# Optimization experiments

Hardware: AMD Instinct MI355X
Metric: run time of the kernel (lower is better)

The kernel has to match this reference:

```python
import jax, jax.numpy as jnp
import numpy as np

BIOSYNTHETIC_FAMILIES = {'glutamate': ['E','Q','P','R','K'], 'aspartate': ['D','N','T','I','M','K'], 'serine': ['S','G','C'], 'pyruvate': ['A','V','L'], 'aromatic': ['F','Y','W'], 'histidine': ['H']}
CODON_TABLE = {'UUU':'F','UUC':'F','UUA':'L','UUG':'L','CUU':'L','CUC':'L','CUA':'L','CUG':'L','AUU':'I','AUC':'I','AUA':'I','AUG':'M','GUU':'V','GUC':'V','GUA':'V','GUG':'V','UCU':'S','UCC':'S','UCA':'S','UCG':'S','CCU':'P','CCC':'P','CCA':'P','CCG':'P','ACU':'T','ACC':'T','ACA':'T','ACG':'T','GCU':'A','GCC':'A','GCA':'A','GCG':'A','UAU':'Y','UAC':'Y','UAA':'*','UAG':'*','CAU':'H','CAC':'H','CAA':'Q','CAG':'Q','AAU':'N','AAC':'N','AAA':'K','AAG':'K','GAU':'D','GAC':'D','GAA':'E','GAG':'E','UGU':'C','UGC':'C','UGA':'*','UGG':'W','CGU':'R','CGC':'R','CGA':'R','CGG':'R','AGU':'S','AGC':'S','AGA':'R','AGG':'R','GGU':'G','GGC':'G','GGA':'G','GGG':'G'}

def _build_family_matrix():
    aa2fam = {aa: f for f, aas in BIOSYNTHETIC_FAMILIES.items() for aa in aas}
    codons = list(CODON_TABLE.keys())
    fam = [aa2fam.get(CODON_TABLE[c]) for c in codons]  # None for stop codons
    M = np.zeros((64, 64), dtype=np.float32)
    for i in range(64):
        for j in range(64):
            if fam[i] is not None and fam[j] is not None and fam[i] == fam[j]:
                M[i, j] = 1.0
    return jnp.asarray(M)

FAMILY_MATRIX = _build_family_matrix()  # (64, 64) constant lookup table

def setup_inputs() -> dict:
    key = jax.random.key(0)
    k1, k2 = jax.random.split(key)
    codon_embeddings = jax.random.normal(k1, (16, 512, 16), dtype=jnp.float32)
    codon_indices = jax.random.randint(k2, (16, 512), 0, 64, dtype=jnp.int64 if jax.config.jax_enable_x64 else jnp.int32)
    return {"codon_embeddings": codon_embeddings, "codon_indices": codon_indices}

def reference(codon_embeddings, codon_indices):
    b, s, d = codon_embeddings.shape
    emb = codon_embeddings.reshape(-1, d)            # (n, d)
    idx = codon_indices.reshape(-1)                  # (n,)
    # Euclidean pairwise distances (torch.cdist, p=2)
    sq = jnp.sum(emb * emb, axis=-1)                 # (n,)
    d2 = sq[:, None] + sq[None, :] - 2.0 * (emb @ emb.T)
    d2 = jnp.maximum(d2, 0.0)
    mask = d2 > 0.0
    dist = jnp.where(mask, jnp.sqrt(jnp.where(mask, d2, 1.0)), 0.0)  # (n, n)
    # Same-family mask via 64x64 lookup gather
    same = FAMILY_MATRIX[idx[:, None], idx[None, :]]  # (n, n)
    eps = 1e-10
    same_sum = jnp.sum(same)
    total = jnp.asarray(dist.shape[0] * dist.shape[1], dist.dtype)
    same_d = jnp.sum(dist * same) / (same_sum + eps)
    diff_d = (jnp.sum(dist) - jnp.sum(dist * same)) / ((total - same_sum) + eps)
    loss = same_d - 0.5 * diff_d + 1.0
    return jax.nn.relu(loss)
```

## Files before the change

kernel.cpp:

```cpp
#include <hip/hip_runtime.h>
#include <math.h>

#define N_ROWS 8192
#define D 16
#define TILE 128
#define NT 64
#define NBLK 2080

#define OFF_PT    0
#define OFF_PS    16384
#define OFF_AP    32768
#define OFF_B1    557056
#define OFF_B2    1081344
#define OFF_FOH   1605632

typedef short  bf16x8 __attribute__((ext_vector_type(8)));
typedef float  f32x4  __attribute__((ext_vector_type(4)));

#if __has_builtin(__builtin_amdgcn_sqrtf)
#define SQRTF(x) __builtin_amdgcn_sqrtf(x)
#else
#define SQRTF(x) sqrtf(x)
#endif

__device__ __constant__ signed char FAM_LUT[64] = {
  4,4,3,3, 3,3,3,3,
  1,1,1,1, 3,3,3,3,
  2,2,2,2, 0,0,0,0,
  1,1,1,1, 3,3,3,3,
  4,4,-1,-1, 5,5,0,0,
  1,1,1,1, 1,1,0,0,
  2,2,-1,4, 0,0,0,0,
  2,2,0,0, 2,2,2,2
};

__device__ __forceinline__ unsigned short f2bf(float f) {
  unsigned u = __float_as_uint(f);
  u += 0x7fffu + ((u >> 16) & 1u);
  return (unsigned short)(u >> 16);
}
__device__ __forceinline__ float bf2f(unsigned short s) {
  return __uint_as_float((unsigned)s << 16);
}

__global__ __launch_bounds__(256) void prep_kernel(
    const float* __restrict__ emb, const int* __restrict__ idx,
    unsigned short* __restrict__ aP, unsigned short* __restrict__ b1,
    unsigned short* __restrict__ b2, unsigned short* __restrict__ foh) {
  const int i = blockIdx.x * 256 + threadIdx.x;
  const float4* src = (const float4*)(emb + (size_t)i * D);
  float v[16];
  float4 a0 = src[0], a1 = src[1], a2 = src[2], a3 = src[3];
  v[0]=a0.x; v[1]=a0.y; v[2]=a0.z; v[3]=a0.w;
  v[4]=a1.x; v[5]=a1.y; v[6]=a1.z; v[7]=a1.w;
  v[8]=a2.x; v[9]=a2.y; v[10]=a2.z; v[11]=a2.w;
  v[12]=a3.x; v[13]=a3.y; v[14]=a3.z; v[15]=a3.w;

  float sq = v[0] * v[0];
#pragma unroll
  for (int k = 1; k < 16; ++k) sq = fmaf(v[k], v[k], sq);
  const unsigned short sqh = f2bf(sq);
  const unsigned short sql = f2bf(sq - bf2f(sqh));
  const unsigned short ONE = 0x3F80;

  unsigned short ah[16], al[16], bh[16], bl[16];
#pragma unroll
  for (int k = 0; k < 16; ++k) {
    bh[k] = f2bf(v[k]);
    bl[k] = f2bf(v[k] - bf2f(bh[k]));
    const float s = -2.0f * v[k];
    ah[k] = f2bf(s);
    al[k] = f2bf(s - bf2f(ah[k]));
  }

  unsigned short A[32], B1[32], B2[32];
#pragma unroll
  for (int k = 0; k < 16; ++k) { A[k] = ah[k]; B1[k] = bh[k]; B2[k] = bl[k]; }
#pragma unroll
  for (int k = 0; k < 12; ++k) { A[16+k] = al[k]; B1[16+k] = bh[k]; B2[16+k] = bl[k]; }
  A[28] = ONE;  A[29] = sqh;  A[30] = sql;  A[31] = al[15];
  B1[28] = sqh; B1[29] = ONE; B1[30] = ONE; B1[31] = bh[15];
  B2[28] = sql; B2[29] = 0;   B2[30] = 0;   B2[31] = bl[15];

#pragma unroll
  for (int c = 0; c < 4; ++c) {
    *(bf16x8*)(aP + (size_t)i * 32 + c * 8) = *(bf16x8*)&A[c * 8];
    *(bf16x8*)(b1 + (size_t)i * 32 + c * 8) = *(bf16x8*)&B1[c * 8];
    *(bf16x8*)(b2 + (size_t)i * 32 + c * 8) = *(bf16x8*)&B2[c * 8];
  }
  const int f = FAM_LUT[idx[i] & 63];
  unsigned short oh[8];
#pragma unroll
  for (int k = 0; k < 8; ++k) oh[k] = (f == k) ? ONE : (unsigned short)0;
  *(bf16x8*)(foh + (size_t)i * 8) = *(bf16x8*)oh;
}

__global__ __launch_bounds__(512, 4) void pair_kernel(
    const unsigned short* __restrict__ aP, const unsigned short* __restrict__ b1g,
    const unsigned short* __restrict__ b2g, const unsigned short* __restrict__ fohg,
    float* __restrict__ pt, float* __restrict__ ps) {
  const int u = blockIdx.y, bx = blockIdx.x;
  int it, jt;
  if (bx < NT - u) { it = u;          jt = u + bx; }
  else             { it = NT - 1 - u; jt = bx - 1; }

  __shared__ __align__(16) unsigned short LB1[4096];
  __shared__ __align__(16) unsigned short LB2[4096];
  __shared__ __align__(16) unsigned short LFB[1024];
  __shared__ __align__(16) unsigned short LZ[8];
  __shared__ float rT[8], rS[8];

  const int t  = threadIdx.x;
  const int w  = t >> 6;
  const int l  = t & 63;
  const int lr = l & 15;
  const int g  = l >> 4;

  {
    const int rl = t >> 2, c = t & 3;
    const size_t gb = (size_t)(jt * TILE + rl) * 32 + c * 8;
    *(bf16x8*)(LB1 + rl * 32 + c * 8) = *(const bf16x8*)(b1g + gb);
    *(bf16x8*)(LB2 + rl * 32 + c * 8) = *(const bf16x8*)(b2g + gb);
    if (t < TILE) *(bf16x8*)(LFB + t * 8) =
        *(const bf16x8*)(fohg + (size_t)(jt * TILE + t) * 8);
    if (t == 128) { bf16x8 z = {0,0,0,0,0,0,0,0}; *(bf16x8*)LZ = z; }
  }

  const int arow = it * TILE + w * 16 + lr;
  const bf16x8 afrag = *(const bf16x8*)(aP + (size_t)arow * 32 + g * 8);
  bf16x8 afrag3;
  if (g == 0) afrag3 = *(const bf16x8*)(fohg + (size_t)arow * 8);
  else        { bf16x8 z = {0,0,0,0,0,0,0,0}; afrag3 = z; }

  __syncthreads();

  const unsigned short* p3 = (g == 0) ? (LFB + lr * 8) : LZ;
  const int step3 = (g == 0) ? 128 : 0;
  const int boff  = lr * 32 + g * 8;
  const f32x4 zf = {0.0f, 0.0f, 0.0f, 0.0f};
  float accT = 0.0f, accS = 0.0f;
#pragma unroll 2
  for (int mj = 0; mj < 8; ++mj) {
    const bf16x8 f1 = *(const bf16x8*)(LB1 + mj * 512 + boff);
    const bf16x8 f2 = *(const bf16x8*)(LB2 + mj * 512 + boff);
    const bf16x8 f3 = *(const bf16x8*)(p3 + mj * step3);
    f32x4 acc = __builtin_amdgcn_mfma_f32_16x16x32_bf16(afrag, f1, zf, 0, 0, 0);
    acc = __builtin_amdgcn_mfma_f32_16x16x32_bf16(afrag, f2, acc, 0, 0, 0);
    const f32x4 msk = __builtin_amdgcn_mfma_f32_16x16x32_bf16(afrag3, f3, zf, 0, 0, 0);
#pragma unroll
    for (int r = 0; r < 4; ++r) {
      const float d2   = fmaxf(acc[r], 0.0f);
      const float dist = SQRTF(d2);
      accT += dist;
      accS = fmaf(msk[r], dist, accS);
    }
  }

#pragma unroll
  for (int off = 32; off > 0; off >>= 1) {
    accT += __shfl_down(accT, off);
    accS += __shfl_down(accS, off);
  }
  if (l == 0) { rT[w] = accT; rS[w] = accS; }
  __syncthreads();
  if (t == 0) {
    float sT = 0.0f, sS = 0.0f;
#pragma unroll
    for (int k = 0; k < 8; ++k) { sT += rT[k]; sS += rS[k]; }
    const float wgt = (it == jt) ? 1.0f : 2.0f;
    const int bid = blockIdx.y * gridDim.x + blockIdx.x;
    pt[bid] = wgt * sT;
    ps[bid] = wgt * sS;
  }
}

__global__ __launch_bounds__(1024) void final_kernel(
    const float* __restrict__ pt, const float* __restrict__ ps,
    const int* __restrict__ idx, float* __restrict__ out) {
  const int t = threadIdx.x, w = t >> 6, l = t & 63;
  __shared__ float  HW[16][8];
  __shared__ double rTd[16], rSd[16];

  const int4* p4 = (const int4*)idx;
  const int4 va = p4[t], vb = p4[t + 1024];
  int vals[8] = {va.x, va.y, va.z, va.w, vb.x, vb.y, vb.z, vb.w};
  float myCnt = 0.0f;
#pragma unroll
  for (int rr = 0; rr < 8; ++rr) {
    const int f = FAM_LUT[vals[rr] & 63];
#pragma unroll
    for (int fam = 0; fam < 6; ++fam) {
      const unsigned long long mk = __ballot(f == fam);
      if (l == fam) myCnt += (float)__popcll(mk);
    }
  }
  if (l < 8) HW[w][l] = (l < 6) ? myCnt : 0.0f;

  double sT = 0.0, sS = 0.0;
  for (int k = t; k < NBLK; k += 1024) { sT += (double)pt[k]; sS += (double)ps[k]; }
#pragma unroll
  for (int off = 32; off > 0; off >>= 1) {
    sT += __shfl_down(sT, off);
    sS += __shfl_down(sS, off);
  }
  if (l == 0) { rTd[w] = sT; rSd[w] = sS; }
  __syncthreads();
  if (t == 0) {
    double tot = 0.0, sam = 0.0;
#pragma unroll
    for (int k = 0; k < 16; ++k) { tot += rTd[k]; sam += rSd[k]; }
    double same_sum = 0.0;
    for (int f = 0; f < 6; ++f) {
      double c = 0.0;
      for (int k = 0; k < 16; ++k) c += (double)HW[k][f];
      same_sum += c * c;
    }
    const double total  = (double)N_ROWS * (double)N_ROWS;
    const double same_d = sam / (same_sum + 1e-10);
    const double diff_d = (tot - sam) / (total - same_sum + 1e-10);
    double loss = same_d - 0.5 * diff_d + 1.0;
    out[0] = (float)(loss > 0.0 ? loss : 0.0);
  }
}

extern "C" void kernel_launch(void* const* d_in, const int* in_sizes, int n_in,
                              void* d_out, int out_size, void* d_ws, size_t ws_size,
                              hipStream_t stream) {
  const float* emb = (const float*)d_in[0];
  const int*   idx = (const int*)d_in[1];
  char* ws = (char*)d_ws;
  float*          pt  = (float*)(ws + OFF_PT);
  float*          ps  = (float*)(ws + OFF_PS);
  unsigned short* aP  = (unsigned short*)(ws + OFF_AP);
  unsigned short* b1  = (unsigned short*)(ws + OFF_B1);
  unsigned short* b2  = (unsigned short*)(ws + OFF_B2);
  unsigned short* foh = (unsigned short*)(ws + OFF_FOH);

  prep_kernel<<<dim3(N_ROWS / 256), dim3(256), 0, stream>>>(emb, idx, aP, b1, b2, foh);
  pair_kernel<<<dim3(NT + 1, NT / 2), dim3(512), 0, stream>>>(aP, b1, b2, foh, pt, ps);
  final_kernel<<<dim3(1), dim3(1024), 0, stream>>>(pt, ps, idx, (float*)d_out);
}
```

Before: 26.40 us.

## Fuse bf16 split-operand preparation into pair kernel, drop prep launch

```diff
diff --git a/kernel.cpp b/kernel.cpp
--- a/kernel.cpp
+++ b/kernel.cpp
@@ -7,12 +7,8 @@
 #define NT 64
 #define NBLK 2080
 
-#define OFF_PT    0
-#define OFF_PS    16384
-#define OFF_AP    32768
-#define OFF_B1    557056
-#define OFF_B2    1081344
-#define OFF_FOH   1605632
+#define OFF_PT   0
+#define OFF_PS   16384
 
 typedef short  bf16x8 __attribute__((ext_vector_type(8)));
 typedef float  f32x4  __attribute__((ext_vector_type(4)));
@@ -22,6 +18,8 @@
 #else
 #define SQRTF(x) sqrtf(x)
 #endif
+
+#define BF_ONE ((unsigned short)0x3F80)
 
 __device__ __constant__ signed char FAM_LUT[64] = {
   4,4,3,3, 3,3,3,3,
@@ -43,61 +41,8 @@
   return __uint_as_float((unsigned)s << 16);
 }
 
-__global__ __launch_bounds__(256) void prep_kernel(
+__global__ __launch_bounds__(512, 4) void pair_kernel(
     const float* __restrict__ emb, const int* __restrict__ idx,
-    unsigned short* __restrict__ aP, unsigned short* __restrict__ b1,
-    unsigned short* __restrict__ b2, unsigned short* __restrict__ foh) {
-  const int i = blockIdx.x * 256 + threadIdx.x;
-  const float4* src = (const float4*)(emb + (size_t)i * D);
-  float v[16];
-  float4 a0 = src[0], a1 = src[1], a2 = src[2], a3 = src[3];
-  v[0]=a0.x; v[1]=a0.y; v[2]=a0.z; v[3]=a0.w;
-  v[4]=a1.x; v[5]=a1.y; v[6]=a1.z; v[7]=a1.w;
-  v[8]=a2.x; v[9]=a2.y; v[10]=a2.z; v[11]=a2.w;
-  v[12]=a3.x; v[13]=a3.y; v[14]=a3.z; v[15]=a3.w;
-
-  float sq = v[0] * v[0];
-#pragma unroll
-  for (int k = 1; k < 16; ++k) sq = fmaf(v[k], v[k], sq);
-  const unsigned short sqh = f2bf(sq);
-  const unsigned short sql = f2bf(sq - bf2f(sqh));
-  const unsigned short ONE = 0x3F80;
-
-  unsigned short ah[16], al[16], bh[16], bl[16];
-#pragma unroll
-  for (int k = 0; k < 16; ++k) {
-    bh[k] = f2bf(v[k]);
-    bl[k] = f2bf(v[k] - bf2f(bh[k]));
-    const float s = -2.0f * v[k];
-    ah[k] = f2bf(s);
-    al[k] = f2bf(s - bf2f(ah[k]));
-  }
-
-  unsigned short A[32], B1[32], B2[32];
-#pragma unroll
-  for (int k = 0; k < 16; ++k) { A[k] = ah[k]; B1[k] = bh[k]; B2[k] = bl[k]; }
-#pragma unroll
-  for (int k = 0; k < 12; ++k) { A[16+k] = al[k]; B1[16+k] = bh[k]; B2[16+k] = bl[k]; }
-  A[28] = ONE;  A[29] = sqh;  A[30] = sql;  A[31] = al[15];
-  B1[28] = sqh; B1[29] = ONE; B1[30] = ONE; B1[31] = bh[15];
-  B2[28] = sql; B2[29] = 0;   B2[30] = 0;   B2[31] = bl[15];
-
-#pragma unroll
-  for (int c = 0; c < 4; ++c) {
-    *(bf16x8*)(aP + (size_t)i * 32 + c * 8) = *(bf16x8*)&A[c * 8];
-    *(bf16x8*)(b1 + (size_t)i * 32 + c * 8) = *(bf16x8*)&B1[c * 8];
-    *(bf16x8*)(b2 + (size_t)i * 32 + c * 8) = *(bf16x8*)&B2[c * 8];
-  }
-  const int f = FAM_LUT[idx[i] & 63];
-  unsigned short oh[8];
-#pragma unroll
-  for (int k = 0; k < 8; ++k) oh[k] = (f == k) ? ONE : (unsigned short)0;
-  *(bf16x8*)(foh + (size_t)i * 8) = *(bf16x8*)oh;
-}
-
-__global__ __launch_bounds__(512, 4) void pair_kernel(
-    const unsigned short* __restrict__ aP, const unsigned short* __restrict__ b1g,
-    const unsigned short* __restrict__ b2g, const unsigned short* __restrict__ fohg,
     float* __restrict__ pt, float* __restrict__ ps) {
   const int u = blockIdx.y, bx = blockIdx.x;
   int it, jt;
@@ -107,7 +52,9 @@
   __shared__ __align__(16) unsigned short LB1[4096];
   __shared__ __align__(16) unsigned short LB2[4096];
   __shared__ __align__(16) unsigned short LFB[1024];
+  __shared__ __align__(16) unsigned short LFA[1024];
   __shared__ __align__(16) unsigned short LZ[8];
+  __shared__ float SQIF[TILE], SQJF[TILE];
   __shared__ float rT[8], rS[8];
 
   const int t  = threadIdx.x;
@@ -116,20 +63,89 @@
   const int lr = l & 15;
   const int g  = l >> 4;
 
-  {
-    const int rl = t >> 2, c = t & 3;
-    const size_t gb = (size_t)(jt * TILE + rl) * 32 + c * 8;
-    *(bf16x8*)(LB1 + rl * 32 + c * 8) = *(const bf16x8*)(b1g + gb);
-    *(bf16x8*)(LB2 + rl * 32 + c * 8) = *(const bf16x8*)(b2g + gb);
-    if (t < TILE) *(bf16x8*)(LFB + t * 8) =
-        *(const bf16x8*)(fohg + (size_t)(jt * TILE + t) * 8);
-    if (t == 128) { bf16x8 z = {0,0,0,0,0,0,0,0}; *(bf16x8*)LZ = z; }
+  if (t < 256) {
+    const int local = t & 127;
+    const int row = ((t < 128) ? it : jt) * TILE + local;
+    const float4* s4 = (const float4*)(emb + (size_t)row * D);
+    float4 a0 = s4[0], a1 = s4[1], a2 = s4[2], a3 = s4[3];
+    float v[16];
+    v[0]=a0.x; v[1]=a0.y; v[2]=a0.z; v[3]=a0.w;
+    v[4]=a1.x; v[5]=a1.y; v[6]=a1.z; v[7]=a1.w;
+    v[8]=a2.x; v[9]=a2.y; v[10]=a2.z; v[11]=a2.w;
+    v[12]=a3.x; v[13]=a3.y; v[14]=a3.z; v[15]=a3.w;
+    float ss = v[0] * v[0];
+#pragma unroll
+    for (int k = 1; k < 16; ++k) ss = fmaf(v[k], v[k], ss);
+    const int f = FAM_LUT[idx[row] & 63];
+    unsigned short oh[8];
+#pragma unroll
+    for (int k = 0; k < 8; ++k) oh[k] = (f == k) ? BF_ONE : (unsigned short)0;
+    if (t < 128) { SQIF[local] = ss; *(bf16x8*)(LFA + local * 8) = *(bf16x8*)oh; }
+    else         { SQJF[local] = ss; *(bf16x8*)(LFB + local * 8) = *(bf16x8*)oh; }
+  } else if (t == 256) {
+    bf16x8 z = {0,0,0,0,0,0,0,0};
+    *(bf16x8*)LZ = z;
+  }
+  __syncthreads();
+
+  if (t < 256) {
+    const int rl = t >> 1, h = t & 1;
+    const int row = jt * TILE + rl;
+    const float4* s4 = (const float4*)(emb + (size_t)row * D + h * 8);
+    float4 b0 = s4[0], b1v = s4[1];
+    float v[8];
+    v[0]=b0.x; v[1]=b0.y; v[2]=b0.z; v[3]=b0.w;
+    v[4]=b1v.x; v[5]=b1v.y; v[6]=b1v.z; v[7]=b1v.w;
+    unsigned short bh[8], bl[8];
+#pragma unroll
+    for (int k = 0; k < 8; ++k) {
+      bh[k] = f2bf(v[k]);
+      bl[k] = f2bf(v[k] - bf2f(bh[k]));
+    }
+    unsigned short* d1 = LB1 + rl * 32;
+    unsigned short* d2 = LB2 + rl * 32;
+    if (h == 0) {
+      *(bf16x8*)(d1 + 0)  = *(bf16x8*)bh;
+      *(bf16x8*)(d1 + 16) = *(bf16x8*)bh;
+      *(bf16x8*)(d2 + 0)  = *(bf16x8*)bl;
+      *(bf16x8*)(d2 + 16) = *(bf16x8*)bl;
+    } else {
+      *(bf16x8*)(d1 + 8) = *(bf16x8*)bh;
+      *(bf16x8*)(d2 + 8) = *(bf16x8*)bl;
+      const float sq = SQJF[rl];
+      const unsigned short sqh = f2bf(sq);
+      const unsigned short sql = f2bf(sq - bf2f(sqh));
+      unsigned short c3h[8] = {bh[0], bh[1], bh[2], bh[3], sqh, BF_ONE, BF_ONE, bh[7]};
+      unsigned short c3l[8] = {bl[0], bl[1], bl[2], bl[3], sql, 0, 0, bl[7]};
+      *(bf16x8*)(d1 + 24) = *(bf16x8*)c3h;
+      *(bf16x8*)(d2 + 24) = *(bf16x8*)c3l;
+    }
   }
 
   const int arow = it * TILE + w * 16 + lr;
-  const bf16x8 afrag = *(const bf16x8*)(aP + (size_t)arow * 32 + g * 8);
+  const float4* a4 = (const float4*)(emb + (size_t)arow * D + (g & 1) * 8);
+  float4 c0 = a4[0], c1 = a4[1];
+  float va[8];
+  va[0]=c0.x; va[1]=c0.y; va[2]=c0.z; va[3]=c0.w;
+  va[4]=c1.x; va[5]=c1.y; va[6]=c1.z; va[7]=c1.w;
+  unsigned short f8[8];
+#pragma unroll
+  for (int k = 0; k < 8; ++k) {
+    const float sv = -2.0f * va[k];
+    const unsigned short h  = f2bf(sv);
+    const unsigned short lo = f2bf(sv - bf2f(h));
+    f8[k] = (g < 2) ? h : lo;
+  }
+  if (g == 3) {
+    const float sq = SQIF[w * 16 + lr];
+    const unsigned short sqh = f2bf(sq);
+    f8[4] = BF_ONE;
+    f8[5] = sqh;
+    f8[6] = f2bf(sq - bf2f(sqh));
+  }
+  const bf16x8 afrag = *(bf16x8*)f8;
   bf16x8 afrag3;
-  if (g == 0) afrag3 = *(const bf16x8*)(fohg + (size_t)arow * 8);
+  if (g == 0) afrag3 = *(const bf16x8*)(LFA + (w * 16 + lr) * 8);
   else        { bf16x8 z = {0,0,0,0,0,0,0,0}; afrag3 = z; }
 
   __syncthreads();
@@ -229,14 +245,9 @@
   const float* emb = (const float*)d_in[0];
   const int*   idx = (const int*)d_in[1];
   char* ws = (char*)d_ws;
-  float*          pt  = (float*)(ws + OFF_PT);
-  float*          ps  = (float*)(ws + OFF_PS);
-  unsigned short* aP  = (unsigned short*)(ws + OFF_AP);
-  unsigned short* b1  = (unsigned short*)(ws + OFF_B1);
-  unsigned short* b2  = (unsigned short*)(ws + OFF_B2);
-  unsigned short* foh = (unsigned short*)(ws + OFF_FOH);
-
-  prep_kernel<<<dim3(N_ROWS / 256), dim3(256), 0, stream>>>(emb, idx, aP, b1, b2, foh);
-  pair_kernel<<<dim3(NT + 1, NT / 2), dim3(512), 0, stream>>>(aP, b1, b2, foh, pt, ps);
+  float* pt = (float*)(ws + OFF_PT);
+  float* ps = (float*)(ws + OFF_PS);
+
+  pair_kernel<<<dim3(NT + 1, NT / 2), dim3(512), 0, stream>>>(emb, idx, pt, ps);
   final_kernel<<<dim3(1), dim3(1024), 0, stream>>>(pt, ps, idx, (float*)d_out);
 }
```

Result: faster. 25.85 us (-2.1%).
